# Kernel optimization log

Hardware: AMD Instinct MI355X
Metric: run time of the kernel (lower is better)

## Reference

```python
import jax, jax.numpy as jnp
import numpy as np

HEADS = 16
LN_EPS = 1e-5


def setup_inputs() -> dict:
    key = jax.random.key(0)
    ks = jax.random.split(key, 4)
    B, S, C, U = 2, 2048, 1024, 1024
    scale = 1.0 / np.sqrt(C)
    return {
        "inputs": jax.random.normal(ks[0], (B, S, C), dtype=jnp.float32),
        "Wq": jax.random.normal(ks[1], (C, U), dtype=jnp.float32) * scale,
        "bq": jnp.zeros((U,), dtype=jnp.float32),
        "Wk": jax.random.normal(ks[2], (C, U), dtype=jnp.float32) * scale,
        "bk": jnp.zeros((U,), dtype=jnp.float32),
        "Wv": jax.random.normal(ks[3], (C, U), dtype=jnp.float32) * scale,
        "bv": jnp.zeros((U,), dtype=jnp.float32),
        "ln_gamma": jnp.ones((S, U), dtype=jnp.float32),
        "ln_beta": jnp.zeros((S, U), dtype=jnp.float32),
    }


def reference(inputs, Wq, bq, Wk, bk, Wv, bv, ln_gamma, ln_beta):
    B, S, C = inputs.shape
    U = Wq.shape[1]
    H = HEADS
    dh = U // H

    Q = inputs @ Wq + bq  # [B,S,U]
    K = inputs @ Wk + bk
    V = inputs @ Wv + bv

    # torch: concat(split(X, U//H, dim=-1), dim=0) -> head-major stacking on batch
    def split_heads(X):
        return jnp.moveaxis(X.reshape(B, S, H, dh), 2, 0).reshape(H * B, S, dh)

    Q_, K_, V_ = split_heads(Q), split_heads(K), split_heads(V)

    scores = jnp.einsum('bqd,bkd->bqk', Q_, K_) / jnp.sqrt(jnp.float32(dh))
    tri = jnp.tril(jnp.ones((S, S), dtype=bool))  # causal mask
    scores = jnp.where(tri[None, :, :], scores, jnp.float32(-1e9))
    attn = jax.nn.softmax(scores, axis=-1)
    out_ = jnp.einsum('bqk,bkd->bqd', attn, V_)  # [H*B,S,dh]

    # inverse: split on batch into H chunks of size B, concat on feature dim
    out = jnp.moveaxis(out_.reshape(H, B, S, dh), 0, 2).reshape(B, S, U)

    out = out + inputs  # residual

    # LayerNorm over normalized_shape=[S, U] (joint seq+feature stats)
    mu = jnp.mean(out, axis=(-2, -1), keepdims=True)
    var = jnp.mean(jnp.square(out - mu), axis=(-2, -1), keepdims=True)
    out = (out - mu) / jnp.sqrt(var + LN_EPS) * ln_gamma + ln_beta
    return out
```

## Files before the change

kernel.cpp:

```cpp
#include <hip/hip_runtime.h>
#include <hip/hip_bf16.h>


typedef __bf16 bf16_t;
typedef __bf16 bf16x8 __attribute__((ext_vector_type(8)));
typedef __bf16 bf16x4 __attribute__((ext_vector_type(4)));
typedef _Float16 f16_t;
typedef _Float16 f16x2 __attribute__((ext_vector_type(2)));
typedef _Float16 f16x4 __attribute__((ext_vector_type(4)));
typedef _Float16 f16x8 __attribute__((ext_vector_type(8)));
typedef float f32x4 __attribute__((ext_vector_type(4)));

constexpr int Bsz = 2;
constexpr int Seq = 2048;
constexpr int Cdim = 1024;
constexpr int Udim = 1024;
constexpr int Hn = 16;
constexpr int Dh = 64;
constexpr int Mrows = Bsz * Seq;
constexpr int PerBatch = Seq * Udim;
constexpr float SCLQ = 0.125f * 1.44269504088896340736f;

__device__ __forceinline__ void gload16(const void* g, void* l)
{
    __builtin_amdgcn_global_load_lds(
        (const __attribute__((address_space(1))) void*)g,
        (__attribute__((address_space(3))) void*)l, 16, 0, 0);
}

__device__ __forceinline__ f16x2 pkrtz(float a, float b)
{
    return __builtin_bit_cast(f16x2, __builtin_amdgcn_cvt_pkrtz(a, b));
}

__global__ __launch_bounds__(256)
void prep(const float* __restrict__ X,
          const float* __restrict__ Wq, const float* __restrict__ Wk,
          const float* __restrict__ Wv,
          bf16_t* __restrict__ Xb,
          bf16_t* __restrict__ Tq, bf16_t* __restrict__ Tk,
          bf16_t* __restrict__ Tv, float* __restrict__ stats)
{
    int z = blockIdx.z;
    int tid = threadIdx.x;
    if (z < 3) {
        const float* W = (z == 0) ? Wq : (z == 1) ? Wk : Wv;
        bf16_t* T = (z == 0) ? Tq : (z == 1) ? Tk : Tv;
        __shared__ bf16_t t[64][65];
        int x0 = blockIdx.x * 64, y0 = blockIdx.y * 64;
        int tx = tid & 63, ty = tid >> 6;
        for (int i = ty; i < 64; i += 4)
            t[i][tx] = (bf16_t)W[(size_t)(y0 + i) * Cdim + x0 + tx];
        __syncthreads();
        for (int i = ty; i < 64; i += 4)
            T[(size_t)(x0 + i) * Cdim + y0 + tx] = t[tx][i];
    } else {
        int bi = blockIdx.y * 16 + blockIdx.x;
        if (bi == 0 && tid < 4) stats[tid] = 0.0f;
        const float4* Xv = (const float4*)X;
#pragma unroll
        for (int k = 0; k < 16; k++) {
            int i = bi * 4096 + k * 256 + tid;
            float4 v = Xv[i];
            bf16x4 o = { (bf16_t)v.x, (bf16_t)v.y, (bf16_t)v.z, (bf16_t)v.w };
            *(bf16x4*)(Xb + (size_t)i * 4) = o;
        }
    }
}

__global__ __launch_bounds__(256)
void gemm_qkv(const bf16_t* __restrict__ X,
              const bf16_t* __restrict__ Wt0, const bf16_t* __restrict__ Wt1,
              const bf16_t* __restrict__ Wt2,
              const float* __restrict__ b0, const float* __restrict__ b1,
              const float* __restrict__ b2,
              f16_t* __restrict__ O0, f16_t* __restrict__ O1, f16_t* __restrict__ O2v)
{
    int z = blockIdx.z;
    const bf16_t* Wt = (z == 0) ? Wt0 : (z == 1) ? Wt1 : Wt2;
    const float* bias = (z == 0) ? b0 : (z == 1) ? b1 : b2;
    float scl = (z == 0) ? SCLQ : 1.0f;

    constexpr int Kd = 1024, Nd = 1024;
    __shared__ __align__(16) bf16_t As[128 * 32];
    __shared__ __align__(16) bf16_t Bs[128 * 32];

    int tid = threadIdx.x;
    int wave = tid >> 6, lane = tid & 63, quad = lane >> 4, l16 = lane & 15;
    int wm = (wave & 1) * 64, wn = (wave >> 1) * 64;
    int m0 = blockIdx.y * 128, n0 = blockIdx.x * 128;

    f32x4 acc[4][4] = {};

    int e0 = wave * 512 + lane * 8;
    int r0 = e0 >> 5, c0 = e0 & 31;
    int e1 = e0 + 2048;
    int r1 = e1 >> 5, c1 = e1 & 31;
    const bf16_t* Ag = X + (size_t)m0 * Kd;
    const bf16_t* Bg = Wt + (size_t)n0 * Kd;
    bf16_t* AsW0 = As + wave * 512;
    bf16_t* AsW1 = As + 2048 + wave * 512;
    bf16_t* BsW0 = Bs + wave * 512;
    bf16_t* BsW1 = Bs + 2048 + wave * 512;

    for (int k0 = 0; k0 < Kd; k0 += 32) {
        gload16(Ag + (size_t)r0 * Kd + k0 + c0, AsW0);
        gload16(Ag + (size_t)r1 * Kd + k0 + c1, AsW1);
        gload16(Bg + (size_t)r0 * Kd + k0 + c0, BsW0);
        gload16(Bg + (size_t)r1 * Kd + k0 + c1, BsW1);
        __syncthreads();

        bf16x8 af[4], bfr[4];
#pragma unroll
        for (int i = 0; i < 4; i++)
            af[i] = *(const bf16x8*)&As[(wm + i * 16 + l16) * 32 + quad * 8];
#pragma unroll
        for (int i = 0; i < 4; i++)
            bfr[i] = *(const bf16x8*)&Bs[(wn + i * 16 + l16) * 32 + quad * 8];
#pragma unroll
        for (int mt = 0; mt < 4; mt++)
#pragma unroll
            for (int nt = 0; nt < 4; nt++)
                acc[mt][nt] = __builtin_amdgcn_mfma_f32_16x16x32_bf16(
                    af[mt], bfr[nt], acc[mt][nt], 0, 0, 0);
        __syncthreads();
    }

    if (z < 2) {
        f16_t* Og = (z == 0) ? O0 : O1;
#pragma unroll
        for (int nt = 0; nt < 4; nt++) {
            int col = n0 + wn + nt * 16 + l16;
            float bv = bias[col];
#pragma unroll
            for (int mt = 0; mt < 4; mt++) {
                int row = m0 + wm + mt * 16 + quad * 4;
#pragma unroll
                for (int r = 0; r < 4; r++)
                    Og[(size_t)(row + r) * Nd + col] = (f16_t)((acc[mt][nt][r] + bv) * scl);
            }
        }
    } else {
        int bb = m0 >> 11;
#pragma unroll
        for (int nt = 0; nt < 4; nt++) {
            int col = n0 + wn + nt * 16 + l16;
            float bv = bias[col];
            int h = col >> 6, d = col & 63;
            f16_t* vbase = O2v + (((size_t)(bb * Hn + h) * Dh + d) << 11);
#pragma unroll
            for (int mt = 0; mt < 4; mt++) {
                int row = m0 + wm + mt * 16 + quad * 4;
                int s = row & (Seq - 1);
                f16x4 pk;
#pragma unroll
                for (int r = 0; r < 4; r++) pk[r] = (f16_t)(acc[mt][nt][r] + bv);
                *(f16x4*)(vbase + s) = pk;
            }
        }
    }
}

__global__ __launch_bounds__(256)
void attn7(const f16_t* __restrict__ Q, const f16_t* __restrict__ K,
           const f16_t* __restrict__ Vt, const float* __restrict__ X,
           bf16_t* __restrict__ R, float* __restrict__ stats)
{
    int id = blockIdx.x;
    int c = id & 7;
    int r8 = id >> 3;
    int g = r8 & 3;
    int kk = r8 >> 2;
    int bh = (g << 3) | c;
    int b = bh >> 4, h = bh & 15;
    int qtile = 31 - kk;

    int tid = threadIdx.x;
    int w = tid >> 6, lane = tid & 63, quad = lane >> 4, l16 = lane & 15;
    size_t bS = (size_t)b * Seq;

    __shared__ f16_t Ks[2][64][72];
    __shared__ f16_t Vs[2][64][72];

    const f16_t* Kg = K + bS * Udim + h * Dh;
    const f16_t* Vg = Vt + ((size_t)(b * Hn + h)) * Dh * Seq;

    int sr = tid >> 2, sc = (tid & 3) * 16;
    int q0 = qtile * 64 + w * 16;
    int qidx = q0 + l16;

    const f16_t* Qp = Q + (bS + qidx) * Udim + h * Dh;
    f16x8 qf[2];
#pragma unroll
    for (int s = 0; s < 2; s++) qf[s] = *(const f16x8*)(Qp + s * 32 + quad * 8);

    f32x4 Oacc[4] = {};
    float lsum = 0.0f;

    const f16_t* kp = Kg + (size_t)sr * Udim + sc;
    const f16_t* vp = Vg + (size_t)sr * Seq + sc;

    {
        f16x8 k0 = *(const f16x8*)kp;
        f16x8 k1 = *(const f16x8*)(kp + 8);
        f16x8 v0 = *(const f16x8*)vp;
        f16x8 v1 = *(const f16x8*)(vp + 8);
        *(f16x8*)&Ks[0][sr][sc] = k0;
        *(f16x8*)&Ks[0][sr][sc + 8] = k1;
        *(f16x8*)&Vs[0][sr][sc] = v0;
        *(f16x8*)&Vs[0][sr][sc + 8] = v1;
        kp += (size_t)64 * Udim;
        vp += 64;
    }
    __syncthreads();

    int buf = 0;
    for (int i = 0; i < qtile; i++) {
        f16x8 nk0 = *(const f16x8*)kp;
        f16x8 nk1 = *(const f16x8*)(kp + 8);
        f16x8 nv0 = *(const f16x8*)vp;
        f16x8 nv1 = *(const f16x8*)(vp + 8);
        kp += (size_t)64 * Udim;
        vp += 64;

        f32x4 st[4];
#pragma unroll
        for (int t = 0; t < 4; t++) {
            f32x4 a = {};
#pragma unroll
            for (int s = 0; s < 2; s++) {
                f16x8 kf = *(const f16x8*)&Ks[buf][t * 16 + l16][s * 32 + quad * 8];
                a = __builtin_amdgcn_mfma_f32_16x16x32_f16(kf, qf[s], a, 0, 0, 0);
            }
            st[t] = a;
        }

        f16x4 pf[4];
#pragma unroll
        for (int t = 0; t < 4; t++) {
            float p0 = exp2f(st[t][0]);
            float p1 = exp2f(st[t][1]);
            float p2 = exp2f(st[t][2]);
            float p3 = exp2f(st[t][3]);
            lsum += (p0 + p1) + (p2 + p3);
            f16x2 lo = pkrtz(p0, p1);
            f16x2 hi = pkrtz(p2, p3);
            pf[t][0] = lo[0]; pf[t][1] = lo[1];
            pf[t][2] = hi[0]; pf[t][3] = hi[1];
        }

#pragma unroll
        for (int t = 0; t < 4; t++)
#pragma unroll
            for (int dt = 0; dt < 4; dt++) {
                f16x4 vf = *(const f16x4*)&Vs[buf][dt * 16 + l16][t * 16 + quad * 4];
                Oacc[dt] = __builtin_amdgcn_mfma_f32_16x16x16f16(vf, pf[t], Oacc[dt], 0, 0, 0);
            }

        *(f16x8*)&Ks[buf ^ 1][sr][sc] = nk0;
        *(f16x8*)&Ks[buf ^ 1][sr][sc + 8] = nk1;
        *(f16x8*)&Vs[buf ^ 1][sr][sc] = nv0;
        *(f16x8*)&Vs[buf ^ 1][sr][sc + 8] = nv1;
        __syncthreads();
        buf ^= 1;
    }

    {
        int kv0 = qtile * 64;
#pragma unroll
        for (int t = 0; t < 4; t++) {
            if (t <= w) {
                f32x4 a = {};
#pragma unroll
                for (int s = 0; s < 2; s++) {
                    f16x8 kf = *(const f16x8*)&Ks[buf][t * 16 + l16][s * 32 + quad * 8];
                    a = __builtin_amdgcn_mfma_f32_16x16x32_f16(kf, qf[s], a, 0, 0, 0);
                }
                f16x4 pfd;
#pragma unroll
                for (int r = 0; r < 4; r++) {
                    float sv = a[r];
                    if (kv0 + t * 16 + quad * 4 + r > qidx) sv = -1e30f;
                    float pv = exp2f(sv);
                    lsum += pv;
                    pfd[r] = (f16_t)pv;
                }
#pragma unroll
                for (int dt = 0; dt < 4; dt++) {
                    f16x4 vf = *(const f16x4*)&Vs[buf][dt * 16 + l16][t * 16 + quad * 4];
                    Oacc[dt] = __builtin_amdgcn_mfma_f32_16x16x16f16(vf, pfd, Oacc[dt], 0, 0, 0);
                }
            }
        }
    }

    lsum += __shfl_xor(lsum, 16);
    lsum += __shfl_xor(lsum, 32);
    float invl = 1.0f / lsum;

    float s_acc = 0.0f, ss_acc = 0.0f;
    const float* Xp = X + (bS + qidx) * Udim + h * Dh;
    bf16_t* Rp = R + (bS + qidx) * Udim + h * Dh;
#pragma unroll
    for (int dt = 0; dt < 4; dt++) {
        f32x4 xv = *(const f32x4*)(Xp + dt * 16 + quad * 4);
        f32x4 o = Oacc[dt] * invl + xv;
        bf16x4 ob;
#pragma unroll
        for (int r = 0; r < 4; r++) {
            ob[r] = (bf16_t)o[r];
            s_acc += o[r];
            ss_acc += o[r] * o[r];
        }
        *(bf16x4*)(Rp + dt * 16 + quad * 4) = ob;
    }

#pragma unroll
    for (int o = 1; o < 64; o <<= 1) {
        s_acc += __shfl_xor(s_acc, o);
        ss_acc += __shfl_xor(ss_acc, o);
    }
    __shared__ float red[8];
    if (lane == 0) { red[w] = s_acc; red[4 + w] = ss_acc; }
    __syncthreads();
    if (tid == 0) {
        atomicAdd(&stats[b], red[0] + red[1] + red[2] + red[3]);
        atomicAdd(&stats[2 + b], red[4] + red[5] + red[6] + red[7]);
    }
}

__global__ __launch_bounds__(256)
void ln_norm(const bf16_t* __restrict__ R, const float* __restrict__ gamma,
             const float* __restrict__ beta, const float* __restrict__ stats,
             float* __restrict__ out)
{
    constexpr float invN = 1.0f / (float)PerBatch;
    float mu[2], inv[2];
#pragma unroll
    for (int b = 0; b < 2; b++) {
        float m = stats[b] * invN;
        float var = stats[2 + b] * invN - m * m;
        mu[b] = m;
        inv[b] = rsqrtf(var + 1e-5f);
    }
    int i = blockIdx.x * 256 + threadIdx.x;
    int f = i * 8;
    int b = f >> 21;
    int su = f & (PerBatch - 1);
    bf16x8 rv = *(const bf16x8*)(R + f);
    float4 g0 = *(const float4*)(gamma + su);
    float4 g1 = *(const float4*)(gamma + su + 4);
    float4 be0 = *(const float4*)(beta + su);
    float4 be1 = *(const float4*)(beta + su + 4);
    float4 o0, o1;
    o0.x = ((float)rv[0] - mu[b]) * inv[b] * g0.x + be0.x;
    o0.y = ((float)rv[1] - mu[b]) * inv[b] * g0.y + be0.y;
    o0.z = ((float)rv[2] - mu[b]) * inv[b] * g0.z + be0.z;
    o0.w = ((float)rv[3] - mu[b]) * inv[b] * g0.w + be0.w;
    o1.x = ((float)rv[4] - mu[b]) * inv[b] * g1.x + be1.x;
    o1.y = ((float)rv[5] - mu[b]) * inv[b] * g1.y + be1.y;
    o1.z = ((float)rv[6] - mu[b]) * inv[b] * g1.z + be1.z;
    o1.w = ((float)rv[7] - mu[b]) * inv[b] * g1.w + be1.w;
    *(float4*)(out + f) = o0;
    *(float4*)(out + f + 4) = o1;
}

extern "C" void kernel_launch(void* const* d_in, const int* in_sizes, int n_in,
                              void* d_out, int out_size, void* d_ws, size_t ws_size,
                              hipStream_t stream)
{
    const float* X     = (const float*)d_in[0];
    const float* Wq    = (const float*)d_in[1];
    const float* bq    = (const float*)d_in[2];
    const float* Wk    = (const float*)d_in[3];
    const float* bk    = (const float*)d_in[4];
    const float* Wv    = (const float*)d_in[5];
    const float* bv    = (const float*)d_in[6];
    const float* gamma = (const float*)d_in[7];
    const float* beta  = (const float*)d_in[8];
    float* out = (float*)d_out;

    char* ws = (char*)d_ws;
    size_t off = 0;
    auto alloc = [&](size_t bytes) -> void* {
        void* p = ws + off;
        off += (bytes + 255) & ~(size_t)255;
        return p;
    };
    bf16_t* Xb = (bf16_t*)alloc((size_t)Mrows * Cdim * 2);
    bf16_t* Tq = (bf16_t*)alloc((size_t)Cdim * Udim * 2);
    bf16_t* Tk = (bf16_t*)alloc((size_t)Cdim * Udim * 2);
    bf16_t* Tv = (bf16_t*)alloc((size_t)Cdim * Udim * 2);
    f16_t*  Qb = (f16_t*)alloc((size_t)Mrows * Udim * 2);
    f16_t*  Kb = (f16_t*)alloc((size_t)Mrows * Udim * 2);
    f16_t*  Vtb = (f16_t*)alloc((size_t)Mrows * Udim * 2);
    bf16_t* Rb = (bf16_t*)alloc((size_t)Mrows * Udim * 2);
    float*  stats = (float*)alloc(4 * sizeof(float));

    prep<<<dim3(16, 16, 4), 256, 0, stream>>>(X, Wq, Wk, Wv, Xb, Tq, Tk, Tv, stats);
    gemm_qkv<<<dim3(8, 32, 3), 256, 0, stream>>>(Xb, Tq, Tk, Tv, bq, bk, bv, Qb, Kb, Vtb);
    attn7<<<dim3(1024), 256, 0, stream>>>(Qb, Kb, Vtb, X, Rb, stats);
    ln_norm<<<dim3(2048), 256, 0, stream>>>(Rb, gamma, beta, stats, out);
}
```

Baseline: 191.5 us.

## Load attention K/V tiles with direct global-to-LDS loads into XOR-swizzled layout

The attention kernel now fetches K and V tiles with global_load_lds straight into shared memory instead of staging them through registers. The padded 72-wide LDS arrays become dense 64-wide tiles with an XOR swizzle on 16-byte chunks to avoid bank conflicts. The loop is unrolled by two with compile-time buffer indices, and exp2 uses the hardware builtin. This is meant to cut register pressure and VALU/LDS-store work, at the cost of more complex indexing and reliance on the async LDS load completing before the barrier.

```diff
diff --git a/kernel.cpp b/kernel.cpp
--- a/kernel.cpp
+++ b/kernel.cpp
@@ -20,6 +20,12 @@
 constexpr int Mrows = Bsz * Seq;
 constexpr int PerBatch = Seq * Udim;
 constexpr float SCLQ = 0.125f * 1.44269504088896340736f;
+
+#if __has_builtin(__builtin_amdgcn_exp2f)
+#define EXP2F(x) __builtin_amdgcn_exp2f(x)
+#else
+#define EXP2F(x) exp2f(x)
+#endif
 
 __device__ __forceinline__ void gload16(const void* g, void* l)
 {
@@ -162,7 +168,7 @@
 }
 
 __global__ __launch_bounds__(256)
-void attn7(const f16_t* __restrict__ Q, const f16_t* __restrict__ K,
+void attn8(const f16_t* __restrict__ Q, const f16_t* __restrict__ K,
            const f16_t* __restrict__ Vt, const float* __restrict__ X,
            bf16_t* __restrict__ R, float* __restrict__ stats)
 {
@@ -179,116 +185,121 @@
     int w = tid >> 6, lane = tid & 63, quad = lane >> 4, l16 = lane & 15;
     size_t bS = (size_t)b * Seq;
 
-    __shared__ f16_t Ks[2][64][72];
-    __shared__ f16_t Vs[2][64][72];
+    __shared__ __align__(16) f16_t Ks[2][4096];
+    __shared__ __align__(16) f16_t Vs[2][4096];
 
     const f16_t* Kg = K + bS * Udim + h * Dh;
     const f16_t* Vg = Vt + ((size_t)(b * Hn + h)) * Dh * Seq;
 
-    int sr = tid >> 2, sc = (tid & 3) * 16;
+    int srow = w * 8 + (lane >> 3);
+    int schunk = (lane & 7) ^ ((lane >> 3) & 7);
+    const f16_t* kp0 = Kg + (size_t)srow * Udim + schunk * 8;
+    const f16_t* kp1 = kp0 + (size_t)32 * Udim;
+    const f16_t* vp0 = Vg + (size_t)srow * Seq + schunk * 8;
+    const f16_t* vp1 = vp0 + (size_t)32 * Seq;
+
     int q0 = qtile * 64 + w * 16;
     int qidx = q0 + l16;
-
     const f16_t* Qp = Q + (bS + qidx) * Udim + h * Dh;
     f16x8 qf[2];
 #pragma unroll
     for (int s = 0; s < 2; s++) qf[s] = *(const f16x8*)(Qp + s * 32 + quad * 8);
 
+    int m = l16 & 7;
+    int kO0 = l16 * 64 + ((quad ^ m) << 3);
+    int kO1 = l16 * 64 + (((4 + quad) ^ m) << 3);
+    int vO[4];
+#pragma unroll
+    for (int t = 0; t < 4; t++)
+        vO[t] = l16 * 64 + (((t * 32 + quad * 8) ^ (m << 4)) >> 1);
+
     f32x4 Oacc[4] = {};
     float lsum = 0.0f;
 
-    const f16_t* kp = Kg + (size_t)sr * Udim + sc;
-    const f16_t* vp = Vg + (size_t)sr * Seq + sc;
+    gload16(kp0, &Ks[0][w * 512]);
+    gload16(kp1, &Ks[0][2048 + w * 512]);
+    gload16(vp0, &Vs[0][w * 512]);
+    gload16(vp1, &Vs[0][2048 + w * 512]);
+    kp0 += (size_t)64 * Udim; kp1 += (size_t)64 * Udim;
+    vp0 += 64; vp1 += 64;
+    __syncthreads();
+
+#define TILE(BUF)                                                              \
+    do {                                                                       \
+               \
+        gload16(kp0, &Ks[(BUF) ^ 1][w * 512]);                                 \
+        gload16(kp1, &Ks[(BUF) ^ 1][2048 + w * 512]);                          \
+        gload16(vp0, &Vs[(BUF) ^ 1][w * 512]);                                 \
+        gload16(vp1, &Vs[(BUF) ^ 1][2048 + w * 512]);                          \
+        kp0 += (size_t)64 * Udim; kp1 += (size_t)64 * Udim;                    \
+        vp0 += 64; vp1 += 64;                                                  \
+        f32x4 st[4];                                                           \
+        _Pragma("unroll")                                                      \
+        for (int t = 0; t < 4; t++) {                                          \
+            f32x4 a = {};                                                      \
+            f16x8 kf0 = *(const f16x8*)&Ks[BUF][kO0 + t * 1024];               \
+            a = __builtin_amdgcn_mfma_f32_16x16x32_f16(kf0, qf[0], a, 0, 0, 0);\
+            f16x8 kf1 = *(const f16x8*)&Ks[BUF][kO1 + t * 1024];               \
+            a = __builtin_amdgcn_mfma_f32_16x16x32_f16(kf1, qf[1], a, 0, 0, 0);\
+            st[t] = a;                                                         \
+        }                                                                      \
+        f16x4 pf[4];                                                           \
+        _Pragma("unroll")                                                      \
+        for (int t = 0; t < 4; t++) {                                          \
+            float p0 = EXP2F(st[t][0]);                                        \
+            float p1 = EXP2F(st[t][1]);                                        \
+            float p2 = EXP2F(st[t][2]);                                        \
+            float p3 = EXP2F(st[t][3]);                                        \
+            lsum += (p0 + p1) + (p2 + p3);                                     \
+            f16x2 lo = pkrtz(p0, p1);                                          \
+            f16x2 hi = pkrtz(p2, p3);                                          \
+            pf[t][0] = lo[0]; pf[t][1] = lo[1];                                \
+            pf[t][2] = hi[0]; pf[t][3] = hi[1];                                \
+        }                                                                      \
+        _Pragma("unroll")                                                      \
+        for (int t = 0; t < 4; t++) {                                          \
+            _Pragma("unroll")                                                  \
+            for (int dt = 0; dt < 4; dt++) {                                   \
+                f16x4 vf = *(const f16x4*)&Vs[BUF][vO[t] + dt * 1024];         \
+                Oacc[dt] = __builtin_amdgcn_mfma_f32_16x16x16f16(              \
+                    vf, pf[t], Oacc[dt], 0, 0, 0);                             \
+            }                                                                  \
+        }                                                                      \
+        __syncthreads();                                                       \
+    } while (0)
 
     {
-        f16x8 k0 = *(const f16x8*)kp;
-        f16x8 k1 = *(const f16x8*)(kp + 8);
-        f16x8 v0 = *(const f16x8*)vp;
-        f16x8 v1 = *(const f16x8*)(vp + 8);
-        *(f16x8*)&Ks[0][sr][sc] = k0;
-        *(f16x8*)&Ks[0][sr][sc + 8] = k1;
-        *(f16x8*)&Vs[0][sr][sc] = v0;
-        *(f16x8*)&Vs[0][sr][sc + 8] = v1;
-        kp += (size_t)64 * Udim;
-        vp += 64;
-    }
-    __syncthreads();
-
-    int buf = 0;
-    for (int i = 0; i < qtile; i++) {
-        f16x8 nk0 = *(const f16x8*)kp;
-        f16x8 nk1 = *(const f16x8*)(kp + 8);
-        f16x8 nv0 = *(const f16x8*)vp;
-        f16x8 nv1 = *(const f16x8*)(vp + 8);
-        kp += (size_t)64 * Udim;
-        vp += 64;
-
-        f32x4 st[4];
-#pragma unroll
-        for (int t = 0; t < 4; t++) {
-            f32x4 a = {};
-#pragma unroll
-            for (int s = 0; s < 2; s++) {
-                f16x8 kf = *(const f16x8*)&Ks[buf][t * 16 + l16][s * 32 + quad * 8];
-                a = __builtin_amdgcn_mfma_f32_16x16x32_f16(kf, qf[s], a, 0, 0, 0);
-            }
-            st[t] = a;
-        }
-
-        f16x4 pf[4];
-#pragma unroll
-        for (int t = 0; t < 4; t++) {
-            float p0 = exp2f(st[t][0]);
-            float p1 = exp2f(st[t][1]);
-            float p2 = exp2f(st[t][2]);
-            float p3 = exp2f(st[t][3]);
-            lsum += (p0 + p1) + (p2 + p3);
-            f16x2 lo = pkrtz(p0, p1);
-            f16x2 hi = pkrtz(p2, p3);
-            pf[t][0] = lo[0]; pf[t][1] = lo[1];
-            pf[t][2] = hi[0]; pf[t][3] = hi[1];
-        }
-
-#pragma unroll
-        for (int t = 0; t < 4; t++)
-#pragma unroll
-            for (int dt = 0; dt < 4; dt++) {
-                f16x4 vf = *(const f16x4*)&Vs[buf][dt * 16 + l16][t * 16 + quad * 4];
-                Oacc[dt] = __builtin_amdgcn_mfma_f32_16x16x16f16(vf, pf[t], Oacc[dt], 0, 0, 0);
-            }
-
-        *(f16x8*)&Ks[buf ^ 1][sr][sc] = nk0;
-        *(f16x8*)&Ks[buf ^ 1][sr][sc + 8] = nk1;
-        *(f16x8*)&Vs[buf ^ 1][sr][sc] = nv0;
-        *(f16x8*)&Vs[buf ^ 1][sr][sc + 8] = nv1;
-        __syncthreads();
-        buf ^= 1;
-    }
+        int i = 0;
+        for (; i + 2 <= qtile; i += 2) { TILE(0); TILE(1); }
+        if (i < qtile) { TILE(0); }
+    }
+#undef TILE
 
     {
+        int dbuf = qtile & 1;
         int kv0 = qtile * 64;
 #pragma unroll
         for (int t = 0; t < 4; t++) {
             if (t <= w) {
                 f32x4 a = {};
-#pragma unroll
-                for (int s = 0; s < 2; s++) {
-                    f16x8 kf = *(const f16x8*)&Ks[buf][t * 16 + l16][s * 32 + quad * 8];
-                    a = __builtin_amdgcn_mfma_f32_16x16x32_f16(kf, qf[s], a, 0, 0, 0);
-                }
+                f16x8 kf0 = *(const f16x8*)&Ks[dbuf][kO0 + t * 1024];
+                a = __builtin_amdgcn_mfma_f32_16x16x32_f16(kf0, qf[0], a, 0, 0, 0);
+                f16x8 kf1 = *(const f16x8*)&Ks[dbuf][kO1 + t * 1024];
+                a = __builtin_amdgcn_mfma_f32_16x16x32_f16(kf1, qf[1], a, 0, 0, 0);
                 f16x4 pfd;
 #pragma unroll
                 for (int r = 0; r < 4; r++) {
                     float sv = a[r];
                     if (kv0 + t * 16 + quad * 4 + r > qidx) sv = -1e30f;
-                    float pv = exp2f(sv);
+                    float pv = EXP2F(sv);
                     lsum += pv;
                     pfd[r] = (f16_t)pv;
                 }
 #pragma unroll
                 for (int dt = 0; dt < 4; dt++) {
-                    f16x4 vf = *(const f16x4*)&Vs[buf][dt * 16 + l16][t * 16 + quad * 4];
-                    Oacc[dt] = __builtin_amdgcn_mfma_f32_16x16x16f16(vf, pfd, Oacc[dt], 0, 0, 0);
+                    f16x4 vf = *(const f16x4*)&Vs[dbuf][vO[t] + dt * 1024];
+                    Oacc[dt] = __builtin_amdgcn_mfma_f32_16x16x16f16(
+                        vf, pfd, Oacc[dt], 0, 0, 0);
                 }
             }
         }
@@ -399,6 +410,6 @@
 
     prep<<<dim3(16, 16, 4), 256, 0, stream>>>(X, Wq, Wk, Wv, Xb, Tq, Tk, Tv, stats);
     gemm_qkv<<<dim3(8, 32, 3), 256, 0, stream>>>(Xb, Tq, Tk, Tv, bq, bk, bv, Qb, Kb, Vtb);
-    attn7<<<dim3(1024), 256, 0, stream>>>(Qb, Kb, Vtb, X, Rb, stats);
+    attn8<<<dim3(1024), 256, 0, stream>>>(Qb, Kb, Vtb, X, Rb, stats);
     ln_norm<<<dim3(2048), 256, 0, stream>>>(Rb, gamma, beta, stats, out);
 }
```

Measured after the change: 186.3 us. 1.03x faster.

## Pair causal query tiles per block, share K/V tiles, async XOR-swizzled LDS loads

Applied to the files above, without the earlier changes.

The attention kernel now gives each block two query tiles, a long one (31-pi) and a short one (pi). They share the K/V tiles staged in LDS, which balances the causal work across blocks and halves the number of K/V tile loads. Staging switches from register round-trips to global_load_lds into an XOR-swizzled unpadded layout, and exp2f is replaced with the hardware exp2 builtin. The grid drops from 1024 to 512 blocks. This lowers parallelism and raises register pressure, since each thread now holds two sets of accumulators.

```diff
diff --git a/kernel.cpp b/kernel.cpp
--- a/kernel.cpp
+++ b/kernel.cpp
@@ -20,6 +20,14 @@
 constexpr int Mrows = Bsz * Seq;
 constexpr int PerBatch = Seq * Udim;
 constexpr float SCLQ = 0.125f * 1.44269504088896340736f;
+
+#if __has_builtin(__builtin_amdgcn_exp2f)
+#define EXP2F(x) __builtin_amdgcn_exp2f(x)
+#else
+#define EXP2F(x) exp2f(x)
+#endif
+
+#define AINL __attribute__((always_inline))
 
 __device__ __forceinline__ void gload16(const void* g, void* l)
 {
@@ -162,157 +170,263 @@
 }
 
 __global__ __launch_bounds__(256)
-void attn7(const f16_t* __restrict__ Q, const f16_t* __restrict__ K,
+void attn9(const f16_t* __restrict__ Q, const f16_t* __restrict__ K,
            const f16_t* __restrict__ Vt, const float* __restrict__ X,
            bf16_t* __restrict__ R, float* __restrict__ stats)
 {
     int id = blockIdx.x;
     int c = id & 7;
-    int r8 = id >> 3;
-    int g = r8 & 3;
-    int kk = r8 >> 2;
+    int r = id >> 3;
+    int g = r & 3;
+    int pi = r >> 2;
     int bh = (g << 3) | c;
     int b = bh >> 4, h = bh & 15;
-    int qtile = 31 - kk;
+    int qa = 31 - pi;
+    int qb = pi;
 
     int tid = threadIdx.x;
     int w = tid >> 6, lane = tid & 63, quad = lane >> 4, l16 = lane & 15;
     size_t bS = (size_t)b * Seq;
 
-    __shared__ f16_t Ks[2][64][72];
-    __shared__ f16_t Vs[2][64][72];
+    __shared__ __align__(16) f16_t Ks[2][4096];
+    __shared__ __align__(16) f16_t Vs[2][4096];
 
     const f16_t* Kg = K + bS * Udim + h * Dh;
     const f16_t* Vg = Vt + ((size_t)(b * Hn + h)) * Dh * Seq;
 
-    int sr = tid >> 2, sc = (tid & 3) * 16;
-    int q0 = qtile * 64 + w * 16;
-    int qidx = q0 + l16;
-
-    const f16_t* Qp = Q + (bS + qidx) * Udim + h * Dh;
-    f16x8 qf[2];
-#pragma unroll
-    for (int s = 0; s < 2; s++) qf[s] = *(const f16x8*)(Qp + s * 32 + quad * 8);
-
-    f32x4 Oacc[4] = {};
-    float lsum = 0.0f;
-
-    const f16_t* kp = Kg + (size_t)sr * Udim + sc;
-    const f16_t* vp = Vg + (size_t)sr * Seq + sc;
-
-    {
-        f16x8 k0 = *(const f16x8*)kp;
-        f16x8 k1 = *(const f16x8*)(kp + 8);
-        f16x8 v0 = *(const f16x8*)vp;
-        f16x8 v1 = *(const f16x8*)(vp + 8);
-        *(f16x8*)&Ks[0][sr][sc] = k0;
-        *(f16x8*)&Ks[0][sr][sc + 8] = k1;
-        *(f16x8*)&Vs[0][sr][sc] = v0;
-        *(f16x8*)&Vs[0][sr][sc + 8] = v1;
-        kp += (size_t)64 * Udim;
-        vp += 64;
-    }
-    __syncthreads();
-
-    int buf = 0;
-    for (int i = 0; i < qtile; i++) {
-        f16x8 nk0 = *(const f16x8*)kp;
-        f16x8 nk1 = *(const f16x8*)(kp + 8);
-        f16x8 nv0 = *(const f16x8*)vp;
-        f16x8 nv1 = *(const f16x8*)(vp + 8);
-        kp += (size_t)64 * Udim;
-        vp += 64;
-
-        f32x4 st[4];
-#pragma unroll
-        for (int t = 0; t < 4; t++) {
+    int srow = w * 8 + (lane >> 3);
+    int schunk = (lane & 7) ^ ((lane >> 3) & 7);
+    const f16_t* kp0 = Kg + (size_t)srow * Udim + schunk * 8;
+    const f16_t* kp1 = kp0 + (size_t)32 * Udim;
+    const f16_t* vp0 = Vg + (size_t)srow * Seq + schunk * 8;
+    const f16_t* vp1 = vp0 + (size_t)32 * Seq;
+
+    int qidxA = qa * 64 + w * 16 + l16;
+    int qidxB = qb * 64 + w * 16 + l16;
+    const f16_t* QpA = Q + (bS + qidxA) * Udim + h * Dh;
+    const f16_t* QpB = Q + (bS + qidxB) * Udim + h * Dh;
+    f16x8 qfA[2], qfB[2];
+#pragma unroll
+    for (int s = 0; s < 2; s++) {
+        qfA[s] = *(const f16x8*)(QpA + s * 32 + quad * 8);
+        qfB[s] = *(const f16x8*)(QpB + s * 32 + quad * 8);
+    }
+
+    int m = l16 & 7;
+    int kO0 = l16 * 64 + ((quad ^ m) << 3);
+    int kO1 = l16 * 64 + (((4 + quad) ^ m) << 3);
+    int vO[4];
+#pragma unroll
+    for (int t = 0; t < 4; t++)
+        vO[t] = l16 * 64 + (((t * 32 + quad * 8) ^ (m << 4)) >> 1);
+
+    f32x4 OA[4] = {}, OB[4] = {};
+    float lsA = 0.0f, lsB = 0.0f;
+
+    auto STAGE = [&](int nb) AINL {
+        gload16(kp0, &Ks[nb][w * 512]);
+        gload16(kp1, &Ks[nb][2048 + w * 512]);
+        gload16(vp0, &Vs[nb][w * 512]);
+        gload16(vp1, &Vs[nb][2048 + w * 512]);
+        kp0 += (size_t)64 * Udim; kp1 += (size_t)64 * Udim;
+        vp0 += 64; vp1 += 64;
+    };
+
+    auto TILE = [&](int buf, bool withB) AINL {
+        STAGE(buf ^ 1);
+        f32x4 stA[4], stB[4];
+#pragma unroll
+        for (int t = 0; t < 4; t++) {
+            f16x8 kf0 = *(const f16x8*)&Ks[buf][kO0 + t * 1024];
+            f16x8 kf1 = *(const f16x8*)&Ks[buf][kO1 + t * 1024];
             f32x4 a = {};
-#pragma unroll
-            for (int s = 0; s < 2; s++) {
-                f16x8 kf = *(const f16x8*)&Ks[buf][t * 16 + l16][s * 32 + quad * 8];
-                a = __builtin_amdgcn_mfma_f32_16x16x32_f16(kf, qf[s], a, 0, 0, 0);
-            }
-            st[t] = a;
-        }
-
-        f16x4 pf[4];
-#pragma unroll
-        for (int t = 0; t < 4; t++) {
-            float p0 = exp2f(st[t][0]);
-            float p1 = exp2f(st[t][1]);
-            float p2 = exp2f(st[t][2]);
-            float p3 = exp2f(st[t][3]);
-            lsum += (p0 + p1) + (p2 + p3);
+            a = __builtin_amdgcn_mfma_f32_16x16x32_f16(kf0, qfA[0], a, 0, 0, 0);
+            a = __builtin_amdgcn_mfma_f32_16x16x32_f16(kf1, qfA[1], a, 0, 0, 0);
+            stA[t] = a;
+            if (withB) {
+                f32x4 bb = {};
+                bb = __builtin_amdgcn_mfma_f32_16x16x32_f16(kf0, qfB[0], bb, 0, 0, 0);
+                bb = __builtin_amdgcn_mfma_f32_16x16x32_f16(kf1, qfB[1], bb, 0, 0, 0);
+                stB[t] = bb;
+            }
+        }
+        f16x4 pA[4], pB[4];
+#pragma unroll
+        for (int t = 0; t < 4; t++) {
+            float p0 = EXP2F(stA[t][0]);
+            float p1 = EXP2F(stA[t][1]);
+            float p2 = EXP2F(stA[t][2]);
+            float p3 = EXP2F(stA[t][3]);
+            lsA += (p0 + p1) + (p2 + p3);
             f16x2 lo = pkrtz(p0, p1);
             f16x2 hi = pkrtz(p2, p3);
-            pf[t][0] = lo[0]; pf[t][1] = lo[1];
-            pf[t][2] = hi[0]; pf[t][3] = hi[1];
-        }
-
-#pragma unroll
-        for (int t = 0; t < 4; t++)
+            pA[t][0] = lo[0]; pA[t][1] = lo[1];
+            pA[t][2] = hi[0]; pA[t][3] = hi[1];
+            if (withB) {
+                float b0 = EXP2F(stB[t][0]);
+                float b1 = EXP2F(stB[t][1]);
+                float b2 = EXP2F(stB[t][2]);
+                float b3 = EXP2F(stB[t][3]);
+                lsB += (b0 + b1) + (b2 + b3);
+                f16x2 blo = pkrtz(b0, b1);
+                f16x2 bhi = pkrtz(b2, b3);
+                pB[t][0] = blo[0]; pB[t][1] = blo[1];
+                pB[t][2] = bhi[0]; pB[t][3] = bhi[1];
+            }
+        }
+#pragma unroll
+        for (int t = 0; t < 4; t++) {
 #pragma unroll
             for (int dt = 0; dt < 4; dt++) {
-                f16x4 vf = *(const f16x4*)&Vs[buf][dt * 16 + l16][t * 16 + quad * 4];
-                Oacc[dt] = __builtin_amdgcn_mfma_f32_16x16x16f16(vf, pf[t], Oacc[dt], 0, 0, 0);
-            }
-
-        *(f16x8*)&Ks[buf ^ 1][sr][sc] = nk0;
-        *(f16x8*)&Ks[buf ^ 1][sr][sc + 8] = nk1;
-        *(f16x8*)&Vs[buf ^ 1][sr][sc] = nv0;
-        *(f16x8*)&Vs[buf ^ 1][sr][sc + 8] = nv1;
+                f16x4 vf = *(const f16x4*)&Vs[buf][vO[t] + dt * 1024];
+                OA[dt] = __builtin_amdgcn_mfma_f32_16x16x16f16(vf, pA[t], OA[dt], 0, 0, 0);
+                if (withB)
+                    OB[dt] = __builtin_amdgcn_mfma_f32_16x16x16f16(vf, pB[t], OB[dt], 0, 0, 0);
+            }
+        }
         __syncthreads();
-        buf ^= 1;
-    }
+    };
+
+    auto TILE_AdB = [&](int buf) AINL {
+        STAGE(buf ^ 1);
+        int kv0 = qb * 64;
+        f32x4 stA[4];
+#pragma unroll
+        for (int t = 0; t < 4; t++) {
+            f16x8 kf0 = *(const f16x8*)&Ks[buf][kO0 + t * 1024];
+            f16x8 kf1 = *(const f16x8*)&Ks[buf][kO1 + t * 1024];
+            f32x4 a = {};
+            a = __builtin_amdgcn_mfma_f32_16x16x32_f16(kf0, qfA[0], a, 0, 0, 0);
+            a = __builtin_amdgcn_mfma_f32_16x16x32_f16(kf1, qfA[1], a, 0, 0, 0);
+            stA[t] = a;
+            if (t <= w) {
+                f32x4 bb = {};
+                bb = __builtin_amdgcn_mfma_f32_16x16x32_f16(kf0, qfB[0], bb, 0, 0, 0);
+                bb = __builtin_amdgcn_mfma_f32_16x16x32_f16(kf1, qfB[1], bb, 0, 0, 0);
+                f16x4 pfd;
+#pragma unroll
+                for (int rr = 0; rr < 4; rr++) {
+                    float sv = bb[rr];
+                    if (kv0 + t * 16 + quad * 4 + rr > qidxB) sv = -1e30f;
+                    float pv = EXP2F(sv);
+                    lsB += pv;
+                    pfd[rr] = (f16_t)pv;
+                }
+#pragma unroll
+                for (int dt = 0; dt < 4; dt++) {
+                    f16x4 vf = *(const f16x4*)&Vs[buf][vO[t] + dt * 1024];
+                    OB[dt] = __builtin_amdgcn_mfma_f32_16x16x16f16(vf, pfd, OB[dt], 0, 0, 0);
+                }
+            }
+        }
+        f16x4 pA[4];
+#pragma unroll
+        for (int t = 0; t < 4; t++) {
+            float p0 = EXP2F(stA[t][0]);
+            float p1 = EXP2F(stA[t][1]);
+            float p2 = EXP2F(stA[t][2]);
+            float p3 = EXP2F(stA[t][3]);
+            lsA += (p0 + p1) + (p2 + p3);
+            f16x2 lo = pkrtz(p0, p1);
+            f16x2 hi = pkrtz(p2, p3);
+            pA[t][0] = lo[0]; pA[t][1] = lo[1];
+            pA[t][2] = hi[0]; pA[t][3] = hi[1];
+        }
+#pragma unroll
+        for (int t = 0; t < 4; t++) {
+#pragma unroll
+            for (int dt = 0; dt < 4; dt++) {
+                f16x4 vf = *(const f16x4*)&Vs[buf][vO[t] + dt * 1024];
+                OA[dt] = __builtin_amdgcn_mfma_f32_16x16x16f16(vf, pA[t], OA[dt], 0, 0, 0);
+            }
+        }
+        __syncthreads();
+    };
+
+    auto DIAG_A = [&](int buf) AINL {
+        int kv0 = qa * 64;
+#pragma unroll
+        for (int t = 0; t < 4; t++) {
+            if (t <= w) {
+                f16x8 kf0 = *(const f16x8*)&Ks[buf][kO0 + t * 1024];
+                f16x8 kf1 = *(const f16x8*)&Ks[buf][kO1 + t * 1024];
+                f32x4 a = {};
+                a = __builtin_amdgcn_mfma_f32_16x16x32_f16(kf0, qfA[0], a, 0, 0, 0);
+                a = __builtin_amdgcn_mfma_f32_16x16x32_f16(kf1, qfA[1], a, 0, 0, 0);
+                f16x4 pfd;
+#pragma unroll
+                for (int rr = 0; rr < 4; rr++) {
+                    float sv = a[rr];
+                    if (kv0 + t * 16 + quad * 4 + rr > qidxA) sv = -1e30f;
+                    float pv = EXP2F(sv);
+                    lsA += pv;
+                    pfd[rr] = (f16_t)pv;
+                }
+#pragma unroll
+                for (int dt = 0; dt < 4; dt++) {
+                    f16x4 vf = *(const f16x4*)&Vs[buf][vO[t] + dt * 1024];
+                    OA[dt] = __builtin_amdgcn_mfma_f32_16x16x16f16(vf, pfd, OA[dt], 0, 0, 0);
+                }
+            }
+        }
+    };
+
+    STAGE(0);
+    __syncthreads();
 
     {
-        int kv0 = qtile * 64;
-#pragma unroll
-        for (int t = 0; t < 4; t++) {
-            if (t <= w) {
-                f32x4 a = {};
-#pragma unroll
-                for (int s = 0; s < 2; s++) {
-                    f16x8 kf = *(const f16x8*)&Ks[buf][t * 16 + l16][s * 32 + quad * 8];
-                    a = __builtin_amdgcn_mfma_f32_16x16x32_f16(kf, qf[s], a, 0, 0, 0);
-                }
-                f16x4 pfd;
-#pragma unroll
-                for (int r = 0; r < 4; r++) {
-                    float sv = a[r];
-                    if (kv0 + t * 16 + quad * 4 + r > qidx) sv = -1e30f;
-                    float pv = exp2f(sv);
-                    lsum += pv;
-                    pfd[r] = (f16_t)pv;
-                }
-#pragma unroll
-                for (int dt = 0; dt < 4; dt++) {
-                    f16x4 vf = *(const f16x4*)&Vs[buf][dt * 16 + l16][t * 16 + quad * 4];
-                    Oacc[dt] = __builtin_amdgcn_mfma_f32_16x16x16f16(vf, pfd, Oacc[dt], 0, 0, 0);
-                }
-            }
-        }
-    }
-
-    lsum += __shfl_xor(lsum, 16);
-    lsum += __shfl_xor(lsum, 32);
-    float invl = 1.0f / lsum;
+        int t = 0;
+        for (; t + 2 <= qb; t += 2) { TILE(0, true); TILE(1, true); }
+        if (t < qb) { TILE(0, true); }
+    }
+    if (qb & 1) TILE_AdB(1); else TILE_AdB(0);
+    {
+        int t = qb + 1;
+        if ((t & 1) && t < qa) { TILE(1, false); t++; }
+        for (; t + 2 <= qa; t += 2) { TILE(0, false); TILE(1, false); }
+        if (t < qa) { TILE(0, false); }
+    }
+    if (qa & 1) DIAG_A(1); else DIAG_A(0);
+
+    lsA += __shfl_xor(lsA, 16);
+    lsA += __shfl_xor(lsA, 32);
+    lsB += __shfl_xor(lsB, 16);
+    lsB += __shfl_xor(lsB, 32);
+    float invA = 1.0f / lsA;
+    float invB = 1.0f / lsB;
 
     float s_acc = 0.0f, ss_acc = 0.0f;
-    const float* Xp = X + (bS + qidx) * Udim + h * Dh;
-    bf16_t* Rp = R + (bS + qidx) * Udim + h * Dh;
+
+    const float* XpA = X + (bS + qidxA) * Udim + h * Dh;
+    bf16_t* RpA = R + (bS + qidxA) * Udim + h * Dh;
 #pragma unroll
     for (int dt = 0; dt < 4; dt++) {
-        f32x4 xv = *(const f32x4*)(Xp + dt * 16 + quad * 4);
-        f32x4 o = Oacc[dt] * invl + xv;
+        f32x4 xv = *(const f32x4*)(XpA + dt * 16 + quad * 4);
+        f32x4 o = OA[dt] * invA + xv;
         bf16x4 ob;
 #pragma unroll
-        for (int r = 0; r < 4; r++) {
-            ob[r] = (bf16_t)o[r];
-            s_acc += o[r];
-            ss_acc += o[r] * o[r];
-        }
-        *(bf16x4*)(Rp + dt * 16 + quad * 4) = ob;
+        for (int rr = 0; rr < 4; rr++) {
+            ob[rr] = (bf16_t)o[rr];
+            s_acc += o[rr];
+            ss_acc += o[rr] * o[rr];
+        }
+        *(bf16x4*)(RpA + dt * 16 + quad * 4) = ob;
+    }
+
+    const float* XpB = X + (bS + qidxB) * Udim + h * Dh;
+    bf16_t* RpB = R + (bS + qidxB) * Udim + h * Dh;
+#pragma unroll
+    for (int dt = 0; dt < 4; dt++) {
+        f32x4 xv = *(const f32x4*)(XpB + dt * 16 + quad * 4);
+        f32x4 o = OB[dt] * invB + xv;
+        bf16x4 ob;
+#pragma unroll
+        for (int rr = 0; rr < 4; rr++) {
+            ob[rr] = (bf16_t)o[rr];
+            s_acc += o[rr];
+            ss_acc += o[rr] * o[rr];
+        }
+        *(bf16x4*)(RpB + dt * 16 + quad * 4) = ob;
     }
 
 #pragma unroll
@@ -399,6 +513,6 @@
 
     prep<<<dim3(16, 16, 4), 256, 0, stream>>>(X, Wq, Wk, Wv, Xb, Tq, Tk, Tv, stats);
     gemm_qkv<<<dim3(8, 32, 3), 256, 0, stream>>>(Xb, Tq, Tk, Tv, bq, bk, bv, Qb, Kb, Vtb);
-    attn7<<<dim3(1024), 256, 0, stream>>>(Qb, Kb, Vtb, X, Rb, stats);
+    attn9<<<dim3(512), 256, 0, stream>>>(Qb, Kb, Vtb, X, Rb, stats);
     ln_norm<<<dim3(2048), 256, 0, stream>>>(Rb, gamma, beta, stats, out);
 }
```

After: 186.3 us. -2.8%, faster.

## Rewrite attention as LDS-free per-wave paired causal strips with fragment-ordered V

Applied to the files above, without the earlier changes.

The attention kernel becomes a 2-wave block in which each wave handles one high and one low 16-row query strip, pairing strips so the causal work per wave is balanced. K and V fragments are loaded straight from global memory into registers with no LDS staging or block barriers, and both strips reuse them. The V-transpose store in the QKV GEMM is rewritten to an MFMA-fragment-ordered layout so those register loads are contiguous. A hardware exp2 builtin replaces exp2f. In exchange, register pressure rises and global/L2 traffic goes up because K/V are no longer shared across waves through LDS.

```diff
diff --git a/kernel.cpp b/kernel.cpp
--- a/kernel.cpp
+++ b/kernel.cpp
@@ -20,6 +20,14 @@
 constexpr int Mrows = Bsz * Seq;
 constexpr int PerBatch = Seq * Udim;
 constexpr float SCLQ = 0.125f * 1.44269504088896340736f;
+
+#if __has_builtin(__builtin_amdgcn_exp2f)
+#define EXP2F(x) __builtin_amdgcn_exp2f(x)
+#else
+#define EXP2F(x) exp2f(x)
+#endif
+
+#define AINL __attribute__((always_inline))
 
 __device__ __forceinline__ void gload16(const void* g, void* l)
 {
@@ -147,164 +155,147 @@
             int col = n0 + wn + nt * 16 + l16;
             float bv = bias[col];
             int h = col >> 6, d = col & 63;
-            f16_t* vbase = O2v + (((size_t)(bb * Hn + h) * Dh + d) << 11);
+            f16_t* vb = O2v + ((size_t)(bb * Hn + h) << 17)
+                            + ((d >> 4) << 8) + ((d & 15) << 4);
 #pragma unroll
             for (int mt = 0; mt < 4; mt++) {
                 int row = m0 + wm + mt * 16 + quad * 4;
                 int s = row & (Seq - 1);
+                int off = ((s >> 6) << 12) + (((s >> 4) & 3) << 10) + (((s >> 2) & 3) << 2);
                 f16x4 pk;
 #pragma unroll
                 for (int r = 0; r < 4; r++) pk[r] = (f16_t)(acc[mt][nt][r] + bv);
-                *(f16x4*)(vbase + s) = pk;
+                *(f16x4*)(vb + off) = pk;
             }
         }
     }
 }
 
-__global__ __launch_bounds__(256)
-void attn7(const f16_t* __restrict__ Q, const f16_t* __restrict__ K,
-           const f16_t* __restrict__ Vt, const float* __restrict__ X,
-           bf16_t* __restrict__ R, float* __restrict__ stats)
+__global__ __launch_bounds__(128, 2)
+void attn11(const f16_t* __restrict__ Q, const f16_t* __restrict__ K,
+            const f16_t* __restrict__ Vt, const float* __restrict__ X,
+            bf16_t* __restrict__ R, float* __restrict__ stats)
 {
     int id = blockIdx.x;
     int c = id & 7;
-    int r8 = id >> 3;
-    int g = r8 & 3;
-    int kk = r8 >> 2;
+    int rest = id >> 3;
+    int g = rest & 3;
+    int pp = rest >> 2;
     int bh = (g << 3) | c;
     int b = bh >> 4, h = bh & 15;
-    int qtile = 31 - kk;
 
     int tid = threadIdx.x;
     int w = tid >> 6, lane = tid & 63, quad = lane >> 4, l16 = lane & 15;
+    int p = pp * 2 + w;
+    int sHi = 127 - p;
+    int sLo = p;
+    int DHi = sHi >> 2;
+    int DLo = sLo >> 2;
+
     size_t bS = (size_t)b * Seq;
-
-    __shared__ f16_t Ks[2][64][72];
-    __shared__ f16_t Vs[2][64][72];
-
-    const f16_t* Kg = K + bS * Udim + h * Dh;
-    const f16_t* Vg = Vt + ((size_t)(b * Hn + h)) * Dh * Seq;
-
-    int sr = tid >> 2, sc = (tid & 3) * 16;
-    int q0 = qtile * 64 + w * 16;
-    int qidx = q0 + l16;
-
-    const f16_t* Qp = Q + (bS + qidx) * Udim + h * Dh;
-    f16x8 qf[2];
-#pragma unroll
-    for (int s = 0; s < 2; s++) qf[s] = *(const f16x8*)(Qp + s * 32 + quad * 8);
-
-    f32x4 Oacc[4] = {};
-    float lsum = 0.0f;
-
-    const f16_t* kp = Kg + (size_t)sr * Udim + sc;
-    const f16_t* vp = Vg + (size_t)sr * Seq + sc;
-
-    {
-        f16x8 k0 = *(const f16x8*)kp;
-        f16x8 k1 = *(const f16x8*)(kp + 8);
-        f16x8 v0 = *(const f16x8*)vp;
-        f16x8 v1 = *(const f16x8*)(vp + 8);
-        *(f16x8*)&Ks[0][sr][sc] = k0;
-        *(f16x8*)&Ks[0][sr][sc + 8] = k1;
-        *(f16x8*)&Vs[0][sr][sc] = v0;
-        *(f16x8*)&Vs[0][sr][sc + 8] = v1;
-        kp += (size_t)64 * Udim;
-        vp += 64;
-    }
-    __syncthreads();
-
-    int buf = 0;
-    for (int i = 0; i < qtile; i++) {
-        f16x8 nk0 = *(const f16x8*)kp;
-        f16x8 nk1 = *(const f16x8*)(kp + 8);
-        f16x8 nv0 = *(const f16x8*)vp;
-        f16x8 nv1 = *(const f16x8*)(vp + 8);
-        kp += (size_t)64 * Udim;
-        vp += 64;
-
-        f32x4 st[4];
+    const f16_t* kbase = K + (bS + l16) * Udim + h * Dh + quad * 8;
+    const f16_t* vbase = Vt + ((size_t)(b * Hn + h) << 17) + l16 * 16 + quad * 4;
+
+    int qiH = sHi * 16 + l16;
+    int qiL = sLo * 16 + l16;
+    const f16_t* QpH = Q + (bS + qiH) * Udim + h * Dh;
+    const f16_t* QpL = Q + (bS + qiL) * Udim + h * Dh;
+    f16x8 qfH[2], qfL[2];
+#pragma unroll
+    for (int s2 = 0; s2 < 2; s2++) {
+        qfH[s2] = *(const f16x8*)(QpH + s2 * 32 + quad * 8);
+        qfL[s2] = *(const f16x8*)(QpL + s2 * 32 + quad * 8);
+    }
+
+    f32x4 OH[4] = {}, OL[4] = {};
+    float lsH = 0.0f, lsL = 0.0f;
+
+    const f16_t* kt = kbase;
+    const f16_t* vtp = vbase;
+
+    auto STRIP = [&](const f16x8 (&kf)[4][2], const f16x4 (&vf)[4][4],
+                     const f16x8 (&qf)[2], f32x4 (&O)[4], float& ls,
+                     int qi, int kv0, int tcap, bool msk) AINL {
 #pragma unroll
         for (int t = 0; t < 4; t++) {
-            f32x4 a = {};
-#pragma unroll
-            for (int s = 0; s < 2; s++) {
-                f16x8 kf = *(const f16x8*)&Ks[buf][t * 16 + l16][s * 32 + quad * 8];
-                a = __builtin_amdgcn_mfma_f32_16x16x32_f16(kf, qf[s], a, 0, 0, 0);
-            }
-            st[t] = a;
-        }
-
-        f16x4 pf[4];
-#pragma unroll
-        for (int t = 0; t < 4; t++) {
-            float p0 = exp2f(st[t][0]);
-            float p1 = exp2f(st[t][1]);
-            float p2 = exp2f(st[t][2]);
-            float p3 = exp2f(st[t][3]);
-            lsum += (p0 + p1) + (p2 + p3);
-            f16x2 lo = pkrtz(p0, p1);
-            f16x2 hi = pkrtz(p2, p3);
-            pf[t][0] = lo[0]; pf[t][1] = lo[1];
-            pf[t][2] = hi[0]; pf[t][3] = hi[1];
-        }
-
-#pragma unroll
-        for (int t = 0; t < 4; t++)
-#pragma unroll
-            for (int dt = 0; dt < 4; dt++) {
-                f16x4 vf = *(const f16x4*)&Vs[buf][dt * 16 + l16][t * 16 + quad * 4];
-                Oacc[dt] = __builtin_amdgcn_mfma_f32_16x16x16f16(vf, pf[t], Oacc[dt], 0, 0, 0);
-            }
-
-        *(f16x8*)&Ks[buf ^ 1][sr][sc] = nk0;
-        *(f16x8*)&Ks[buf ^ 1][sr][sc + 8] = nk1;
-        *(f16x8*)&Vs[buf ^ 1][sr][sc] = nv0;
-        *(f16x8*)&Vs[buf ^ 1][sr][sc + 8] = nv1;
-        __syncthreads();
-        buf ^= 1;
-    }
-
-    {
-        int kv0 = qtile * 64;
-#pragma unroll
-        for (int t = 0; t < 4; t++) {
-            if (t <= w) {
+            if (t <= tcap) {
                 f32x4 a = {};
-#pragma unroll
-                for (int s = 0; s < 2; s++) {
-                    f16x8 kf = *(const f16x8*)&Ks[buf][t * 16 + l16][s * 32 + quad * 8];
-                    a = __builtin_amdgcn_mfma_f32_16x16x32_f16(kf, qf[s], a, 0, 0, 0);
-                }
-                f16x4 pfd;
+                a = __builtin_amdgcn_mfma_f32_16x16x32_f16(kf[t][0], qf[0], a, 0, 0, 0);
+                a = __builtin_amdgcn_mfma_f32_16x16x32_f16(kf[t][1], qf[1], a, 0, 0, 0);
+                float pv[4];
 #pragma unroll
                 for (int r = 0; r < 4; r++) {
                     float sv = a[r];
-                    if (kv0 + t * 16 + quad * 4 + r > qidx) sv = -1e30f;
-                    float pv = exp2f(sv);
-                    lsum += pv;
-                    pfd[r] = (f16_t)pv;
+                    if (msk && (kv0 + t * 16 + quad * 4 + r > qi)) sv = -1e30f;
+                    pv[r] = EXP2F(sv);
+                    ls += pv[r];
                 }
-#pragma unroll
-                for (int dt = 0; dt < 4; dt++) {
-                    f16x4 vf = *(const f16x4*)&Vs[buf][dt * 16 + l16][t * 16 + quad * 4];
-                    Oacc[dt] = __builtin_amdgcn_mfma_f32_16x16x16f16(vf, pfd, Oacc[dt], 0, 0, 0);
-                }
+                f16x2 lo = pkrtz(pv[0], pv[1]);
+                f16x2 hi = pkrtz(pv[2], pv[3]);
+                f16x4 pf;
+                pf[0] = lo[0]; pf[1] = lo[1]; pf[2] = hi[0]; pf[3] = hi[1];
+#pragma unroll
+                for (int dt = 0; dt < 4; dt++)
+                    O[dt] = __builtin_amdgcn_mfma_f32_16x16x16f16(vf[t][dt], pf, O[dt], 0, 0, 0);
             }
         }
-    }
-
-    lsum += __shfl_xor(lsum, 16);
-    lsum += __shfl_xor(lsum, 32);
-    float invl = 1.0f / lsum;
+    };
+
+    for (int t64 = 0; t64 < DHi; t64++) {
+        f16x8 kf[4][2];
+        f16x4 vf[4][4];
+#pragma unroll
+        for (int t = 0; t < 4; t++)
+#pragma unroll
+            for (int s2 = 0; s2 < 2; s2++)
+                kf[t][s2] = *(const f16x8*)(kt + (size_t)t * 16 * Udim + s2 * 32);
+#pragma unroll
+        for (int t = 0; t < 4; t++)
+#pragma unroll
+            for (int dt = 0; dt < 4; dt++)
+                vf[t][dt] = *(const f16x4*)(vtp + t * 1024 + dt * 256);
+
+        int kv0 = t64 << 6;
+        STRIP(kf, vf, qfH, OH, lsH, qiH, kv0, 3, false);
+        if (t64 < DLo)
+            STRIP(kf, vf, qfL, OL, lsL, qiL, kv0, 3, false);
+        else if (t64 == DLo)
+            STRIP(kf, vf, qfL, OL, lsL, qiL, kv0, sLo & 3, true);
+
+        kt += (size_t)64 * Udim;
+        vtp += 4096;
+    }
+    {
+        f16x8 kf[4][2];
+        f16x4 vf[4][4];
+#pragma unroll
+        for (int t = 0; t < 4; t++)
+#pragma unroll
+            for (int s2 = 0; s2 < 2; s2++)
+                kf[t][s2] = *(const f16x8*)(kt + (size_t)t * 16 * Udim + s2 * 32);
+#pragma unroll
+        for (int t = 0; t < 4; t++)
+#pragma unroll
+            for (int dt = 0; dt < 4; dt++)
+                vf[t][dt] = *(const f16x4*)(vtp + t * 1024 + dt * 256);
+        STRIP(kf, vf, qfH, OH, lsH, qiH, DHi << 6, sHi & 3, true);
+    }
+
+    lsH += __shfl_xor(lsH, 16);
+    lsH += __shfl_xor(lsH, 32);
+    lsL += __shfl_xor(lsL, 16);
+    lsL += __shfl_xor(lsL, 32);
+    float invH = 1.0f / lsH;
+    float invL = 1.0f / lsL;
 
     float s_acc = 0.0f, ss_acc = 0.0f;
-    const float* Xp = X + (bS + qidx) * Udim + h * Dh;
-    bf16_t* Rp = R + (bS + qidx) * Udim + h * Dh;
+
+    const float* XpH = X + (bS + qiH) * Udim + h * Dh;
+    bf16_t* RpH = R + (bS + qiH) * Udim + h * Dh;
 #pragma unroll
     for (int dt = 0; dt < 4; dt++) {
-        f32x4 xv = *(const f32x4*)(Xp + dt * 16 + quad * 4);
-        f32x4 o = Oacc[dt] * invl + xv;
+        f32x4 xv = *(const f32x4*)(XpH + dt * 16 + quad * 4);
+        f32x4 o = OH[dt] * invH + xv;
         bf16x4 ob;
 #pragma unroll
         for (int r = 0; r < 4; r++) {
@@ -312,7 +303,23 @@
             s_acc += o[r];
             ss_acc += o[r] * o[r];
         }
-        *(bf16x4*)(Rp + dt * 16 + quad * 4) = ob;
+        *(bf16x4*)(RpH + dt * 16 + quad * 4) = ob;
+    }
+
+    const float* XpL = X + (bS + qiL) * Udim + h * Dh;
+    bf16_t* RpL = R + (bS + qiL) * Udim + h * Dh;
+#pragma unroll
+    for (int dt = 0; dt < 4; dt++) {
+        f32x4 xv = *(const f32x4*)(XpL + dt * 16 + quad * 4);
+        f32x4 o = OL[dt] * invL + xv;
+        bf16x4 ob;
+#pragma unroll
+        for (int r = 0; r < 4; r++) {
+            ob[r] = (bf16_t)o[r];
+            s_acc += o[r];
+            ss_acc += o[r] * o[r];
+        }
+        *(bf16x4*)(RpL + dt * 16 + quad * 4) = ob;
     }
 
 #pragma unroll
@@ -320,12 +327,12 @@
         s_acc += __shfl_xor(s_acc, o);
         ss_acc += __shfl_xor(ss_acc, o);
     }
-    __shared__ float red[8];
-    if (lane == 0) { red[w] = s_acc; red[4 + w] = ss_acc; }
+    __shared__ float red[4];
+    if (lane == 0) { red[w] = s_acc; red[2 + w] = ss_acc; }
     __syncthreads();
     if (tid == 0) {
-        atomicAdd(&stats[b], red[0] + red[1] + red[2] + red[3]);
-        atomicAdd(&stats[2 + b], red[4] + red[5] + red[6] + red[7]);
+        atomicAdd(&stats[b], red[0] + red[1]);
+        atomicAdd(&stats[2 + b], red[2] + red[3]);
     }
 }
 
@@ -399,6 +406,6 @@
 
     prep<<<dim3(16, 16, 4), 256, 0, stream>>>(X, Wq, Wk, Wv, Xb, Tq, Tk, Tv, stats);
     gemm_qkv<<<dim3(8, 32, 3), 256, 0, stream>>>(Xb, Tq, Tk, Tv, bq, bk, bv, Qb, Kb, Vtb);
-    attn7<<<dim3(1024), 256, 0, stream>>>(Qb, Kb, Vtb, X, Rb, stats);
+    attn11<<<dim3(1024), 128, 0, stream>>>(Qb, Kb, Vtb, X, Rb, stats);
     ln_norm<<<dim3(2048), 256, 0, stream>>>(Rb, gamma, beta, stats, out);
 }
```

New measurement: 240.4 us. +25.5%, slower.
